# Kernel optimization log

Hardware: AMD Instinct MI355X
Metric: run time of the kernel (lower is better)

The kernel has to match this reference:

```python
import jax, jax.numpy as jnp
import numpy as np

B, N, C_IN, C_OUT, K = 8, 4096, 64, 128, 15
RADIUS = 0.1            # 2.5 * grid_size(0.04) * sigma(1.0)
MAX_NN = 34
KP_EXTENT = 0.04        # point_influence = prev_grid_size * sigma
KERNEL_RADIUS = 1.5 * KP_EXTENT
NEG_SLOPE = 0.2
BN_EPS = 1e-5


def setup_inputs() -> dict:
    key = jax.random.key(0)
    k1, k2, k3, k4 = jax.random.split(key, 4)
    xyz = jax.random.uniform(k1, (B, N, 3), dtype=jnp.float32)
    feats = jax.random.normal(k2, (B, N, C_IN), dtype=jnp.float32)
    # fixed kernel point disposition inside the kernel ball (requires_grad=False in torch)
    kp = jax.random.normal(k3, (K, 3), dtype=jnp.float32)
    kp = kp / (jnp.linalg.norm(kp, axis=-1, keepdims=True) + 1e-6) * KERNEL_RADIUS * 0.7
    kp = kp.at[0].set(0.0)  # center point
    std = float(np.sqrt(2.0 / (K * C_IN)))
    weight = jax.random.normal(k4, (K, C_IN, C_OUT), dtype=jnp.float32) * std
    gamma = jnp.ones((C_OUT,), dtype=jnp.float32)
    beta = jnp.zeros((C_OUT,), dtype=jnp.float32)
    return {"xyz": xyz, "feats": feats, "K_points": kp, "weight": weight,
            "gamma": gamma, "beta": beta}


def _ball_query(xyz):
    # xyz: [B, N, 3] -> flat neighbor idx [B*N, MAX_NN] into the concatenated
    # point array; missing neighbors get shadow index B*N.
    b_, n_, _ = xyz.shape
    shadow = b_ * n_

    def per_cloud(pts, b):
        d2 = jnp.sum((pts[:, None, :] - pts[None, :, :]) ** 2, axis=-1)  # [N, N]
        neg_d2, idx = jax.lax.top_k(-d2, MAX_NN)                         # k nearest
        valid = (-neg_d2) <= RADIUS ** 2
        return jnp.where(valid, idx + b * n_, shadow)

    return jax.vmap(per_cloud)(xyz, jnp.arange(b_)).reshape(b_ * n_, MAX_NN)


def _kpconv_block(xyz, feats, K_points, weight, gamma, beta):
    b_, n_, _ = xyz.shape
    pts = xyz.reshape(b_ * n_, 3)
    f = feats.reshape(b_ * n_, C_IN)
    nidx = _ball_query(xyz)                                   # [M, nn]
    # shadow point far away / zero features (KPConv_ops)
    pts_pad = jnp.concatenate([pts, jnp.full((1, 3), 1e6, pts.dtype)], axis=0)
    f_pad = jnp.concatenate([f, jnp.zeros((1, C_IN), f.dtype)], axis=0)
    nbr = pts_pad[nidx] - pts[:, None, :]                     # [M, nn, 3] relative coords
    sq = jnp.sum((nbr[:, :, None, :] - K_points) ** 2, -1)    # [M, nn, K]
    w = jnp.maximum(1.0 - jnp.sqrt(sq) / KP_EXTENT, 0.0)      # linear influence
    nf = f_pad[nidx]                                          # [M, nn, Cin]
    wf = jnp.einsum('mnk,mnc->mkc', w, nf)                    # per-kernel-point feats
    out = jnp.einsum('mkc,kcd->md', wf, weight)               # [M, Cout]
    # FastBatchNorm1d (training-mode batch stats, biased var) + LeakyReLU
    mu = out.mean(axis=0)
    var = out.var(axis=0)
    out = (out - mu) * jax.lax.rsqrt(var + BN_EPS) * gamma + beta
    out = jnp.where(out >= 0, out, NEG_SLOPE * out)
    return out.reshape(b_, n_, C_OUT)


def reference(xyz, feats, K_points, weight, gamma, beta):
    return _kpconv_block(xyz, feats, K_points, weight, gamma, beta)
```

## Files before the change

kernel.cpp:

```cpp
#include <hip/hip_runtime.h>


#define NB     8
#define NPTS   4096
#define M_TOT  32768
#define CIN    64
#define COUT   128
#define NKP    15
#define NCELL  1728
#define MAXROWS 64
#define UCAP   512
#define R2EFF  (0.082f * 0.082f)
#define KP_INV 25.0f
#define NEG_SLOPE 0.2f
#define KCP    1024
#define WFPAD  1032
#define SP     40

typedef float f32x4_t __attribute__((ext_vector_type(4)));
typedef short bf16x8_t __attribute__((ext_vector_type(8)));

__device__ __forceinline__ unsigned short f2bf(float f) {
  union { float f; unsigned u; } v; v.f = f;
  unsigned r = v.u + 0x7FFF + ((v.u >> 16) & 1);
  return (unsigned short)(r >> 16);
}
__device__ __forceinline__ int cell_of(float x, float y, float z) {
  int cx = (int)(x * 12.f); cx = cx > 11 ? 11 : cx;
  int cy = (int)(y * 12.f); cy = cy > 11 ? 11 : cy;
  int cz = (int)(z * 12.f); cz = cz > 11 ? 11 : cz;
  return (cz * 12 + cy) * 12 + cx;
}

__global__ __launch_bounds__(256) void k0a_hist(
    const float* __restrict__ xyz, int* __restrict__ cellcnt)
{
  const int pt = blockIdx.x * 256 + threadIdx.x;
  const float x = xyz[pt * 3], y = xyz[pt * 3 + 1], z = xyz[pt * 3 + 2];
  const int b = pt >> 12;
  atomicAdd(&cellcnt[b * NCELL + cell_of(x, y, z)], 1);
}

__global__ __launch_bounds__(256) void k0b_scan_kW(
    const int* __restrict__ cellcnt, int* __restrict__ cellstart,
    const float* __restrict__ W, unsigned short* __restrict__ Wt)
{
  if (blockIdx.x >= 8) {
    const int idx = (blockIdx.x - 8) * 256 + threadIdx.x;
    const int d = idx & 127, c = idx >> 7;
    union { unsigned short s[16]; uint4 v[2]; } u;
    #pragma unroll
    for (int k = 0; k < NKP; k++)
      u.s[k] = f2bf(W[(size_t)k * (CIN * COUT) + c * COUT + d]);
    u.s[15] = 0;
    uint4* dst = (uint4*)&Wt[(size_t)d * KCP + c * 16];
    dst[0] = u.v[0]; dst[1] = u.v[1];
    return;
  }
  __shared__ int ps[256];
  const int b = blockIdx.x, t = threadIdx.x;
  int local[7], s = 0;
  #pragma unroll
  for (int i = 0; i < 7; i++) {
    const int cid = t * 7 + i;
    const int c = (cid < NCELL) ? cellcnt[b * NCELL + cid] : 0;
    local[i] = c; s += c;
  }
  ps[t] = s; __syncthreads();
  for (int off = 1; off < 256; off <<= 1) {
    int v = (t >= off) ? ps[t - off] : 0;
    __syncthreads();
    ps[t] += v;
    __syncthreads();
  }
  int run = ps[t] - s;
  #pragma unroll
  for (int i = 0; i < 7; i++) {
    const int cid = t * 7 + i;
    if (cid < NCELL) { cellstart[b * 1729 + cid] = run; run += local[i]; }
  }
  if (t == 255) cellstart[b * 1729 + NCELL] = ps[255];
}

__global__ __launch_bounds__(256) void k0c_scatter(
    const float* __restrict__ xyz, const int* __restrict__ cellstart,
    int* __restrict__ cellfill, int* __restrict__ qorder,
    float4* __restrict__ xyzs)
{
  const int pt = blockIdx.x * 256 + threadIdx.x;
  const float x = xyz[pt * 3], y = xyz[pt * 3 + 1], z = xyz[pt * 3 + 2];
  const int b = pt >> 12;
  const int cid = cell_of(x, y, z);
  const int slot = atomicAdd(&cellfill[b * NCELL + cid], 1);
  const int pos = b * NPTS + cellstart[b * 1729 + cid] + slot;
  qorder[pos] = pt;
  xyzs[pos] = make_float4(x, y, z, 0.f);
}

__global__ __launch_bounds__(256, 3) void k2_conv(
    const float4* __restrict__ xyzs, const float* __restrict__ feats,
    const float* __restrict__ kpts, const int* __restrict__ cellstart,
    const int* __restrict__ qorder, const unsigned short* __restrict__ Wt,
    float* __restrict__ out, float* __restrict__ psum,
    float* __restrict__ psumsq)
{
  __shared__ char smraw[33792] __attribute__((aligned(16)));
  float4*         Pu   = (float4*)smraw;
  unsigned short* cpos = (unsigned short*)(smraw + 8192);
  short (*S)[SP]       = (short(*)[SP])(smraw + 8192);
  short (*FT)[SP]      = (short(*)[SP])(smraw + 28672);
  short (*wf)[WFPAD]   = (short(*)[WFPAD])smraw;

  __shared__ float4 qd[16];
  __shared__ int    qm[16];
  __shared__ float  kp[NKP][4];
  __shared__ int    rowrs[MAXROWS], rowlen[MAXROWS], pfx[MAXROWS + 1];
  __shared__ int    meta[6];
  __shared__ int    ucnt;

  const int tid = threadIdx.x;
  const int w   = tid >> 6;
  const int L   = tid & 63;
  const int m0  = blockIdx.x * 16;
  const int b   = m0 >> 12;

  if (tid < NKP * 3) {
    int k = tid / 3, c = tid - k * 3;
    kp[k][c] = kpts[tid];
  }
  if (tid < 16) {
    qd[tid] = xyzs[m0 + tid];
    qm[tid] = qorder[m0 + tid];
  }
  if (tid == 32) ucnt = 0;
  __syncthreads();

  if (tid == 0) {
    int x0 = 12, x1 = -1, y0 = 12, y1 = -1, z0 = 12, z1 = -1;
    for (int i = 0; i < 16; i++) {
      const float4 Q = qd[i];
      int cx = (int)(Q.x * 12.f); cx = cx > 11 ? 11 : cx;
      int cy = (int)(Q.y * 12.f); cy = cy > 11 ? 11 : cy;
      int cz = (int)(Q.z * 12.f); cz = cz > 11 ? 11 : cz;
      x0 = cx < x0 ? cx : x0; x1 = cx > x1 ? cx : x1;
      y0 = cy < y0 ? cy : y0; y1 = cy > y1 ? cy : y1;
      z0 = cz < z0 ? cz : z0; z1 = cz > z1 ? cz : z1;
    }
    x0 = x0 > 0 ? x0 - 1 : 0;  x1 = x1 < 11 ? x1 + 1 : 11;
    y0 = y0 > 0 ? y0 - 1 : 0;  y1 = y1 < 11 ? y1 + 1 : 11;
    z0 = z0 > 0 ? z0 - 1 : 0;  z1 = z1 < 11 ? z1 + 1 : 11;
    int nr = (y1 - y0 + 1) * (z1 - z0 + 1);
    meta[0] = y0; meta[1] = y1 - y0 + 1; meta[2] = z0;
    meta[3] = x0; meta[4] = x1;
    meta[5] = nr > MAXROWS ? MAXROWS : nr;
  }
  __syncthreads();

  const int nrows = meta[5], yspan = meta[1];
  if (tid < nrows) {
    const int z = meta[2] + tid / yspan, y = meta[0] + tid % yspan;
    const int base = b * 1729 + (z * 12 + y) * 12;
    const int rs = cellstart[base + meta[3]];
    rowrs[tid]  = rs;
    rowlen[tid] = cellstart[base + meta[4] + 1] - rs;
  }
  __syncthreads();
  if (tid == 0) {
    int run = 0;
    for (int r = 0; r < nrows; r++) { pfx[r] = run; run += rowlen[r]; }
    pfx[nrows] = run;
  }
  __syncthreads();
  if (tid < nrows) {
    const int rs = rowrs[tid], len = rowlen[tid], o = pfx[tid];
    for (int i = 0; i < len; i++) cpos[o + i] = (unsigned short)(rs + i);
  }
  __syncthreads();
  const int T = pfx[nrows];

  for (int tb = 0; tb < T; tb += 256) {
    const int t = tb + tid;
    if (t < T) {
      const int pos = (int)cpos[t];
      const float4 P = xyzs[b * NPTS + pos];
      float best = 1e9f;
      #pragma unroll
      for (int i = 0; i < 16; i++) {
        const float4 Q = qd[i];
        const float dx = P.x - Q.x, dy = P.y - Q.y, dz = P.z - Q.z;
        best = fminf(best, dx * dx + dy * dy + dz * dz);
      }
      if (best <= R2EFF) {
        const int slot = atomicAdd(&ucnt, 1);
        if (slot < UCAP)
          Pu[slot] = make_float4(P.x, P.y, P.z, __int_as_float(pos));
      }
    }
  }
  __syncthreads();
  int U = ucnt; U = U > UCAP ? UCAP : U;

  const int ln = L & 15;
  const int kh = L >> 4;

  f32x4_t acc[16];
  #pragma unroll
  for (int mt = 0; mt < 16; mt++) acc[mt] = (f32x4_t){0.f, 0.f, 0.f, 0.f};

  for (int ub = 0; ub < U; ub += 32) {
    {
      const int c  = tid & 63;
      const int i0 = tid >> 6;
      #pragma unroll
      for (int ii = 0; ii < 8; ii++) {
        const int i = ii * 4 + i0;
        const int u = ub + i;
        short v = 0;
        if (u < U) {
          const int pos  = __float_as_int(Pu[u].w);
          const int orig = qorder[b * NPTS + pos];
          v = (short)f2bf(feats[(size_t)orig * CIN + c]);
        }
        FT[c][i] = v;
      }
    }
    #pragma unroll
    for (int rep = 0; rep < 2; rep++) {
      const int p = rep * 256 + tid;
      const int q = p >> 5;
      const int n = p & 31;
      const int u = ub + n;
      if (u < U) {
        const float4 P = Pu[u];
        const float4 Q = qd[q];
        const float rx = P.x - Q.x, ry = P.y - Q.y, rz = P.z - Q.z;
        #pragma unroll
        for (int k = 0; k < NKP; k++) {
          const float dx = rx - kp[k][0];
          const float dy = ry - kp[k][1];
          const float dz = rz - kp[k][2];
          const float wv =
              fmaxf(1.f - sqrtf(dx * dx + dy * dy + dz * dz) * KP_INV, 0.f);
          S[q * 16 + k][n] = (short)f2bf(wv);
        }
        S[q * 16 + 15][n] = 0;
      } else {
        #pragma unroll
        for (int k = 0; k < 16; k++) S[q * 16 + k][n] = 0;
      }
    }
    __syncthreads();

    bf16x8_t bb = *(const bf16x8_t*)&FT[w * 16 + ln][kh * 8];
    #pragma unroll
    for (int mt = 0; mt < 16; mt++) {
      bf16x8_t aa = *(const bf16x8_t*)&S[mt * 16 + ln][kh * 8];
      acc[mt] = __builtin_amdgcn_mfma_f32_16x16x32_bf16(aa, bb, acc[mt],
                                                        0, 0, 0);
    }
    __syncthreads();
  }

  #pragma unroll
  for (int mt = 0; mt < 16; mt++) {
    union { unsigned short s[4]; unsigned long long d; } u;
    #pragma unroll
    for (int j = 0; j < 4; j++) u.s[j] = f2bf(acc[mt][j]);
    *(unsigned long long*)&wf[mt][(w * 16 + ln) * 16 + kh * 4] = u.d;
  }
  __syncthreads();

  const int colbase = w * 32;

  f32x4_t acc2[2];
  acc2[0] = (f32x4_t){0.f, 0.f, 0.f, 0.f};
  acc2[1] = (f32x4_t){0.f, 0.f, 0.f, 0.f};

  const unsigned short* Bp0 = &Wt[(size_t)(colbase + ln) * KCP + kh * 8];
  const unsigned short* Bp1 = Bp0 + 16 * KCP;
  const short* Ap = &wf[ln][kh * 8];

  #pragma unroll 4
  for (int kk = 0; kk < 32; kk++) {
    const int ko = kk * 32;
    bf16x8_t b0 = *(const bf16x8_t*)(Bp0 + ko);
    bf16x8_t b1 = *(const bf16x8_t*)(Bp1 + ko);
    bf16x8_t a0 = *(const bf16x8_t*)(Ap + ko);
    acc2[0] = __builtin_amdgcn_mfma_f32_16x16x32_bf16(a0, b0, acc2[0], 0, 0, 0);
    acc2[1] = __builtin_amdgcn_mfma_f32_16x16x32_bf16(a0, b1, acc2[1], 0, 0, 0);
  }

  float s0 = 0.f, q0 = 0.f, s1 = 0.f, q1 = 0.f;
  #pragma unroll
  for (int j = 0; j < 4; j++) {
    s0 += acc2[0][j]; q0 += acc2[0][j] * acc2[0][j];
    s1 += acc2[1][j]; q1 += acc2[1][j] * acc2[1][j];
  }
  s0 += __shfl_xor(s0, 16); s0 += __shfl_xor(s0, 32);
  q0 += __shfl_xor(q0, 16); q0 += __shfl_xor(q0, 32);
  s1 += __shfl_xor(s1, 16); s1 += __shfl_xor(s1, 32);
  q1 += __shfl_xor(q1, 16); q1 += __shfl_xor(q1, 32);
  if (kh == 0) {
    atomicAdd(&psum[colbase + ln], s0);
    atomicAdd(&psumsq[colbase + ln], q0);
    atomicAdd(&psum[colbase + 16 + ln], s1);
    atomicAdd(&psumsq[colbase + 16 + ln], q1);
  }

  #pragma unroll
  for (int c = 0; c < 2; c++) {
    #pragma unroll
    for (int j = 0; j < 4; j++) {
      const int row = kh * 4 + j;
      out[(size_t)qm[row] * COUT + colbase + c * 16 + ln] = acc2[c][j];
    }
  }
}

__global__ __launch_bounds__(256) void k4_norm(
    float* __restrict__ out, const float* __restrict__ psum,
    const float* __restrict__ psumsq, const float* __restrict__ gamma,
    const float* __restrict__ beta)
{
  __shared__ float a_s[128], b_s[128];
  if (threadIdx.x < 128) {
    const int d = threadIdx.x;
    double mu  = (double)psum[d] / (double)M_TOT;
    double var = (double)psumsq[d] / (double)M_TOT - mu * mu;
    float rstd = (float)(1.0 / sqrt(var + 1e-5));
    float a = rstd * gamma[d];
    a_s[d] = a;
    b_s[d] = beta[d] - (float)mu * a;
  }
  __syncthreads();
  const int idx = blockIdx.x * 256 + threadIdx.x;
  float4 v = ((const float4*)out)[idx];
  const int d0 = (idx * 4) & 127;
  float y0 = v.x * a_s[d0 + 0] + b_s[d0 + 0];
  float y1 = v.y * a_s[d0 + 1] + b_s[d0 + 1];
  float y2 = v.z * a_s[d0 + 2] + b_s[d0 + 2];
  float y3 = v.w * a_s[d0 + 3] + b_s[d0 + 3];
  v.x = y0 >= 0.f ? y0 : NEG_SLOPE * y0;
  v.y = y1 >= 0.f ? y1 : NEG_SLOPE * y1;
  v.z = y2 >= 0.f ? y2 : NEG_SLOPE * y2;
  v.w = y3 >= 0.f ? y3 : NEG_SLOPE * y3;
  ((float4*)out)[idx] = v;
}

extern "C" void kernel_launch(void* const* d_in, const int* in_sizes, int n_in,
                              void* d_out, int out_size, void* d_ws,
                              size_t ws_size, hipStream_t stream)
{
  const float* xyz   = (const float*)d_in[0];
  const float* feats = (const float*)d_in[1];
  const float* kpts  = (const float*)d_in[2];
  const float* W     = (const float*)d_in[3];
  const float* gamma = (const float*)d_in[4];
  const float* beta  = (const float*)d_in[5];
  float* out = (float*)d_out;

  char* ws = (char*)d_ws;
  int*            cellcnt   = (int*)(ws + 0);
  int*            cellfill  = (int*)(ws + 55296);
  float*          psum      = (float*)(ws + 110592);
  float*          psumsq    = (float*)(ws + 111104);
  int*            cellstart = (int*)(ws + 111616);
  int*            qorder    = (int*)(ws + 167040);
  float4*         xyzs      = (float4*)(ws + 298112);
  unsigned short* Wt        = (unsigned short*)(ws + 822400);

  hipMemsetAsync(ws, 0, 111616, stream);

  k0a_hist   <<< 128, 256, 0, stream>>>(xyz, cellcnt);
  k0b_scan_kW<<<  40, 256, 0, stream>>>(cellcnt, cellstart, W, Wt);
  k0c_scatter<<< 128, 256, 0, stream>>>(xyz, cellstart, cellfill, qorder,
                                        xyzs);
  k2_conv    <<<2048, 256, 0, stream>>>(xyzs, feats, kpts, cellstart, qorder,
                                        Wt, out, psum, psumsq);
  k4_norm    <<<(out_size / 4) / 256, 256, 0, stream>>>(out, psum, psumsq,
                                                        gamma, beta);
}
```

Measured before the change: 202.7 us.

## Pre-sort features to bf16 in scatter, wave-level setup, raise occupancy

The scatter kernel now writes a copy of the features in cell-sorted order, already converted to bf16. The conv kernel then gathers them directly, with no qorder indirection and no per-element float-to-bf16 conversion. The conv block setup (bounding box, row prefix sum, cpos fill) moves from serial thread-0 loops plus several barriers to a single wavefront using shuffles, and launch bounds rise to 4 blocks per SM. This costs an extra 4 MB workspace write and read, and the occupancy hint may force register spills.

```diff
diff --git a/kernel.cpp b/kernel.cpp
--- a/kernel.cpp
+++ b/kernel.cpp
@@ -8,7 +8,6 @@
 #define COUT   128
 #define NKP    15
 #define NCELL  1728
-#define MAXROWS 64
 #define UCAP   512
 #define R2EFF  (0.082f * 0.082f)
 #define KP_INV 25.0f
@@ -83,9 +82,10 @@
 }
 
 __global__ __launch_bounds__(256) void k0c_scatter(
-    const float* __restrict__ xyz, const int* __restrict__ cellstart,
-    int* __restrict__ cellfill, int* __restrict__ qorder,
-    float4* __restrict__ xyzs)
+    const float* __restrict__ xyz, const float* __restrict__ feats,
+    const int* __restrict__ cellstart, int* __restrict__ cellfill,
+    int* __restrict__ qorder, float4* __restrict__ xyzs,
+    unsigned short* __restrict__ fsorted)
 {
   const int pt = blockIdx.x * 256 + threadIdx.x;
   const float x = xyz[pt * 3], y = xyz[pt * 3 + 1], z = xyz[pt * 3 + 2];
@@ -95,10 +95,21 @@
   const int pos = b * NPTS + cellstart[b * 1729 + cid] + slot;
   qorder[pos] = pt;
   xyzs[pos] = make_float4(x, y, z, 0.f);
-}
-
-__global__ __launch_bounds__(256, 3) void k2_conv(
-    const float4* __restrict__ xyzs, const float* __restrict__ feats,
+  const float* src = &feats[(size_t)pt * CIN];
+  uint4* dst = (uint4*)&fsorted[(size_t)pos * CIN];
+  #pragma unroll
+  for (int g = 0; g < 8; g++) {
+    float4 a = *(const float4*)(src + g * 8);
+    float4 c = *(const float4*)(src + g * 8 + 4);
+    union { unsigned short s[8]; uint4 v; } u;
+    u.s[0] = f2bf(a.x); u.s[1] = f2bf(a.y); u.s[2] = f2bf(a.z); u.s[3] = f2bf(a.w);
+    u.s[4] = f2bf(c.x); u.s[5] = f2bf(c.y); u.s[6] = f2bf(c.z); u.s[7] = f2bf(c.w);
+    dst[g] = u.v;
+  }
+}
+
+__global__ __launch_bounds__(256, 4) void k2_conv(
+    const float4* __restrict__ xyzs, const unsigned short* __restrict__ fsorted,
     const float* __restrict__ kpts, const int* __restrict__ cellstart,
     const int* __restrict__ qorder, const unsigned short* __restrict__ Wt,
     float* __restrict__ out, float* __restrict__ psum,
@@ -114,8 +125,7 @@
   __shared__ float4 qd[16];
   __shared__ int    qm[16];
   __shared__ float  kp[NKP][4];
-  __shared__ int    rowrs[MAXROWS], rowlen[MAXROWS], pfx[MAXROWS + 1];
-  __shared__ int    meta[6];
+  __shared__ int    Tsh;
   __shared__ int    ucnt;
 
   const int tid = threadIdx.x;
@@ -124,59 +134,63 @@
   const int m0  = blockIdx.x * 16;
   const int b   = m0 >> 12;
 
-  if (tid < NKP * 3) {
-    int k = tid / 3, c = tid - k * 3;
-    kp[k][c] = kpts[tid];
-  }
-  if (tid < 16) {
-    qd[tid] = xyzs[m0 + tid];
-    qm[tid] = qorder[m0 + tid];
-  }
-  if (tid == 32) ucnt = 0;
+  if (tid >= 64 && tid < 64 + NKP * 3) {
+    const int t2 = tid - 64;
+    kp[t2 / 3][t2 - (t2 / 3) * 3] = kpts[t2];
+  }
+
+  if (tid < 64) {
+    int cxm = 12, cym = 12, czm = 12, cxM = -1, cyM = -1, czM = -1;
+    if (tid < 16) {
+      const float4 Q = xyzs[m0 + tid];
+      qd[tid] = Q;
+      qm[tid] = qorder[m0 + tid];
+      int a = (int)(Q.x * 12.f); a = a > 11 ? 11 : a;
+      int c = (int)(Q.y * 12.f); c = c > 11 ? 11 : c;
+      int d = (int)(Q.z * 12.f); d = d > 11 ? 11 : d;
+      cxm = cxM = a; cym = cyM = c; czm = czM = d;
+    }
+    #pragma unroll
+    for (int off = 8; off >= 1; off >>= 1) {
+      int v;
+      v = __shfl_xor(cxm, off); cxm = v < cxm ? v : cxm;
+      v = __shfl_xor(cxM, off); cxM = v > cxM ? v : cxM;
+      v = __shfl_xor(cym, off); cym = v < cym ? v : cym;
+      v = __shfl_xor(cyM, off); cyM = v > cyM ? v : cyM;
+      v = __shfl_xor(czm, off); czm = v < czm ? v : czm;
+      v = __shfl_xor(czM, off); czM = v > czM ? v : czM;
+    }
+    cxm = __shfl(cxm, 0); cxM = __shfl(cxM, 0);
+    cym = __shfl(cym, 0); cyM = __shfl(cyM, 0);
+    czm = __shfl(czm, 0); czM = __shfl(czM, 0);
+
+    const int x0 = cxm > 0 ? cxm - 1 : 0, x1 = cxM < 11 ? cxM + 1 : 11;
+    const int y0 = cym > 0 ? cym - 1 : 0, y1 = cyM < 11 ? cyM + 1 : 11;
+    const int z0 = czm > 0 ? czm - 1 : 0, z1 = czM < 11 ? czM + 1 : 11;
+    const int yspan = y1 - y0 + 1;
+    int nr = yspan * (z1 - z0 + 1);
+    nr = nr > 64 ? 64 : nr;
+
+    int rs = 0, len = 0;
+    if (tid < nr) {
+      const int zz = z0 + tid / yspan, yy = y0 + tid % yspan;
+      const int base = b * 1729 + (zz * 12 + yy) * 12;
+      rs  = cellstart[base + x0];
+      len = cellstart[base + x1 + 1] - rs;
+    }
+    int incl = len;
+    #pragma unroll
+    for (int off = 1; off < 64; off <<= 1) {
+      const int v = __shfl_up(incl, off);
+      if (tid >= off) incl += v;
+    }
+    const int excl = incl - len;
+    for (int i = 0; i < len; i++) cpos[excl + i] = (unsigned short)(rs + i);
+    if (tid == 63) Tsh = incl;
+    if (tid == 62) ucnt = 0;
+  }
   __syncthreads();
-
-  if (tid == 0) {
-    int x0 = 12, x1 = -1, y0 = 12, y1 = -1, z0 = 12, z1 = -1;
-    for (int i = 0; i < 16; i++) {
-      const float4 Q = qd[i];
-      int cx = (int)(Q.x * 12.f); cx = cx > 11 ? 11 : cx;
-      int cy = (int)(Q.y * 12.f); cy = cy > 11 ? 11 : cy;
-      int cz = (int)(Q.z * 12.f); cz = cz > 11 ? 11 : cz;
-      x0 = cx < x0 ? cx : x0; x1 = cx > x1 ? cx : x1;
-      y0 = cy < y0 ? cy : y0; y1 = cy > y1 ? cy : y1;
-      z0 = cz < z0 ? cz : z0; z1 = cz > z1 ? cz : z1;
-    }
-    x0 = x0 > 0 ? x0 - 1 : 0;  x1 = x1 < 11 ? x1 + 1 : 11;
-    y0 = y0 > 0 ? y0 - 1 : 0;  y1 = y1 < 11 ? y1 + 1 : 11;
-    z0 = z0 > 0 ? z0 - 1 : 0;  z1 = z1 < 11 ? z1 + 1 : 11;
-    int nr = (y1 - y0 + 1) * (z1 - z0 + 1);
-    meta[0] = y0; meta[1] = y1 - y0 + 1; meta[2] = z0;
-    meta[3] = x0; meta[4] = x1;
-    meta[5] = nr > MAXROWS ? MAXROWS : nr;
-  }
-  __syncthreads();
-
-  const int nrows = meta[5], yspan = meta[1];
-  if (tid < nrows) {
-    const int z = meta[2] + tid / yspan, y = meta[0] + tid % yspan;
-    const int base = b * 1729 + (z * 12 + y) * 12;
-    const int rs = cellstart[base + meta[3]];
-    rowrs[tid]  = rs;
-    rowlen[tid] = cellstart[base + meta[4] + 1] - rs;
-  }
-  __syncthreads();
-  if (tid == 0) {
-    int run = 0;
-    for (int r = 0; r < nrows; r++) { pfx[r] = run; run += rowlen[r]; }
-    pfx[nrows] = run;
-  }
-  __syncthreads();
-  if (tid < nrows) {
-    const int rs = rowrs[tid], len = rowlen[tid], o = pfx[tid];
-    for (int i = 0; i < len; i++) cpos[o + i] = (unsigned short)(rs + i);
-  }
-  __syncthreads();
-  const int T = pfx[nrows];
+  const int T = Tsh;
 
   for (int tb = 0; tb < T; tb += 256) {
     const int t = tb + tid;
@@ -188,7 +202,8 @@
       for (int i = 0; i < 16; i++) {
         const float4 Q = qd[i];
         const float dx = P.x - Q.x, dy = P.y - Q.y, dz = P.z - Q.z;
-        best = fminf(best, dx * dx + dy * dy + dz * dz);
+        const float d2 = dx * dx + dy * dy + dz * dz;
+        best = d2 < best ? d2 : best;
       }
       if (best <= R2EFF) {
         const int slot = atomicAdd(&ucnt, 1);
@@ -217,9 +232,8 @@
         const int u = ub + i;
         short v = 0;
         if (u < U) {
-          const int pos  = __float_as_int(Pu[u].w);
-          const int orig = qorder[b * NPTS + pos];
-          v = (short)f2bf(feats[(size_t)orig * CIN + c]);
+          const int pos = __float_as_int(Pu[u].w);
+          v = (short)fsorted[(size_t)(b * NPTS + pos) * CIN + c];
         }
         FT[c][i] = v;
       }
@@ -367,16 +381,17 @@
   int*            cellstart = (int*)(ws + 111616);
   int*            qorder    = (int*)(ws + 167040);
   float4*         xyzs      = (float4*)(ws + 298112);
-  unsigned short* Wt        = (unsigned short*)(ws + 822400);
+  unsigned short* fsorted   = (unsigned short*)(ws + 822400);
+  unsigned short* Wt        = (unsigned short*)(ws + 5016704);
 
   hipMemsetAsync(ws, 0, 111616, stream);
 
   k0a_hist   <<< 128, 256, 0, stream>>>(xyz, cellcnt);
   k0b_scan_kW<<<  40, 256, 0, stream>>>(cellcnt, cellstart, W, Wt);
-  k0c_scatter<<< 128, 256, 0, stream>>>(xyz, cellstart, cellfill, qorder,
-                                        xyzs);
-  k2_conv    <<<2048, 256, 0, stream>>>(xyzs, feats, kpts, cellstart, qorder,
-                                        Wt, out, psum, psumsq);
+  k0c_scatter<<< 128, 256, 0, stream>>>(xyz, feats, cellstart, cellfill,
+                                        qorder, xyzs, fsorted);
+  k2_conv    <<<2048, 256, 0, stream>>>(xyzs, fsorted, kpts, cellstart,
+                                        qorder, Wt, out, psum, psumsq);
   k4_norm    <<<(out_size / 4) / 256, 256, 0, stream>>>(out, psum, psumsq,
                                                         gamma, beta);
 }
```

Result: faster. 196.5 us (-3.0%).
